# Kernel optimization log

Measured on AMD Instinct MI355X. Metric: run time of the kernel, lower is better.

The kernel has to match this reference:

```python
import jax, jax.numpy as jnp
import numpy as np

SE_TEMP = 0.2
BN_EPS = 1e-5

def _l2n(x):
    # F.normalize(p=2, dim=-1) with eps=1e-12 clamp on the norm
    n = jnp.linalg.norm(x, axis=-1, keepdims=True)
    return x / jnp.maximum(n, 1e-12)

def setup_inputs() -> dict:
    key = jax.random.key(0)
    k1, k2, k3, k4, k5 = jax.random.split(key, 5)
    Q, I, D = 256, 2048, 256
    return {
        "query_feats": jax.random.normal(k1, (Q, D), dtype=jnp.float32),
        "query_img_feats": jax.random.normal(k2, (Q, D), dtype=jnp.float32),
        "gallery_img_feats": jax.random.normal(k3, (I, D), dtype=jnp.float32),
        "bn_gamma": jnp.ones((D,), dtype=jnp.float32),
        "bn_beta": jnp.zeros((D,), dtype=jnp.float32),
        "bn_mean": jax.random.normal(k4, (D,), dtype=jnp.float32) * 0.1,
        "bn_var": jax.random.uniform(k5, (D,), dtype=jnp.float32, minval=0.5, maxval=1.5),
    }

def reference(query_feats, query_img_feats, gallery_img_feats, bn_gamma, bn_beta, bn_mean, bn_var):
    # GalleryFilterNetwork.get_scores, mode='combined', gfn_activation_mode='se'
    inv_std = bn_gamma / jnp.sqrt(bn_var + BN_EPS)

    def bn(x):  # eval-mode BatchNorm1d over last dim D
        return (x - bn_mean) * inv_std + bn_beta

    xq = _l2n(query_feats)        # [Q, D] normalized query box feats
    yq = _l2n(query_img_feats)    # [Q, D] normalized query scene feats
    yg = _l2n(gallery_img_feats)  # [I, D] normalized gallery scene feats

    gate = jax.nn.sigmoid(xq / SE_TEMP)           # [Q, D]
    fused_query = bn(yq * gate)                   # [Q, D]  (non-p SE fuse)
    fused_gal = bn(yg[:, None, :] * gate[None])   # [I, Q, D] (p=True SE fuse)

    # cosine similarity per (q, i) pair, then sigmoid
    scores = jax.nn.sigmoid(
        jnp.einsum('qd,iqd->qi', _l2n(fused_query), _l2n(fused_gal))
    )
    return scores  # [Q, I]
```

## Files before the change

kernel.cpp:

```cpp
#include <hip/hip_runtime.h>
#include <math.h>

#define D 256
#define Q 256
#define I 2048

typedef __attribute__((ext_vector_type(8))) short short8;
typedef __attribute__((ext_vector_type(4))) float floatx4;

__device__ __forceinline__ float sigmoidf_(float x) {
    return 1.0f / (1.0f + expf(-x));
}

__device__ __forceinline__ unsigned short f2bf(float f) {
    unsigned u = __float_as_uint(f);
    u += 0x7FFFu + ((u >> 16) & 1u);
    return (unsigned short)(u >> 16);
}

__device__ __forceinline__ float quad_sum(float v) {
    v += __shfl_xor(v, 16, 64);
    v += __shfl_xor(v, 32, 64);
    return v;
}

#define LOAD8(dst, src4, base)                                      \
    do {                                                            \
        float4 _a = (src4)[(base)];                                 \
        float4 _b = (src4)[(base) + 1];                             \
        (dst)[0] = _a.x; (dst)[1] = _a.y;                           \
        (dst)[2] = _a.z; (dst)[3] = _a.w;                           \
        (dst)[4] = _b.x; (dst)[5] = _b.y;                           \
        (dst)[6] = _b.z; (dst)[7] = _b.w;                           \
    } while (0)

__global__ void __launch_bounds__(64, 1)
gfn_one(const float* __restrict__ qf,
        const float* __restrict__ qif,
        const float* __restrict__ gal,
        const float* __restrict__ gamma,
        const float* __restrict__ beta,
        const float* __restrict__ mean,
        const float* __restrict__ var,
        float* __restrict__ out) {
    const int l = threadIdx.x;
    const int lm = l & 15, quad = l >> 4;
    const int q0 = blockIdx.x * 16, i0 = blockIdx.y * 32;
    const int qr = q0 + lm;
    const int cb = quad * 2;

    const float4* qf4  = (const float4*)qf;
    const float4* qif4 = (const float4*)qif;
    const float4* g4   = (const float4*)gal;
    const float4* ga4  = (const float4*)gamma;
    const float4* be4  = (const float4*)beta;
    const float4* me4  = (const float4*)mean;
    const float4* va4  = (const float4*)var;

    float xx[64];
#pragma unroll
    for (int ks = 0; ks < 8; ks++)
        LOAD8(&xx[ks * 8], qf4, qr * 64 + ks * 8 + cb);
    float nx = 0.f;
#pragma unroll
    for (int e = 0; e < 64; e++) nx += xx[e] * xx[e];
    nx = quad_sum(nx);
    const float inx = 1.0f / fmaxf(sqrtf(nx), 1e-12f);
#pragma unroll
    for (int e = 0; e < 64; e++) xx[e] = sigmoidf_(xx[e] * inx * 5.0f);

    float yy[64];
#pragma unroll
    for (int ks = 0; ks < 8; ks++)
        LOAD8(&yy[ks * 8], qif4, qr * 64 + ks * 8 + cb);
    float ny = 0.f;
#pragma unroll
    for (int e = 0; e < 64; e++) ny += yy[e] * yy[e];
    ny = quad_sum(ny);
    const float iny = 1.0f / fmaxf(sqrtf(ny), 1e-12f);

    float cc_[64];
#pragma unroll
    for (int ks = 0; ks < 8; ks++) {
        float pg[8], pb_[8], pm[8], pv[8];
        LOAD8(pg, ga4, ks * 8 + cb);
        LOAD8(pb_, be4, ks * 8 + cb);
        LOAD8(pm, me4, ks * 8 + cb);
        LOAD8(pv, va4, ks * 8 + cb);
#pragma unroll
        for (int e = 0; e < 8; e++) {
            const int j = ks * 8 + e;
            float is = pg[e] * rsqrtf(pv[e] + 1e-5f);
            float c = pb_[e] - pm[e] * is;
            float a = xx[j] * is;
            xx[j] = a;
            yy[j] = yy[j] * iny * a + c;
            cc_[j] = c;
        }
    }

    float nf = 0.f;
#pragma unroll
    for (int e = 0; e < 64; e++) nf += yy[e] * yy[e];
    nf = quad_sum(nf);
    const float inf_ = 1.0f / fmaxf(sqrtf(nf), 1e-12f);

    float s = 0.f, ccs = 0.f;
#pragma unroll
    for (int e = 0; e < 64; e++) {
        float u = yy[e] * inf_;
        s += u * cc_[e];
        ccs += cc_[e] * cc_[e];
    }
    const float sqv = quad_sum(s);
    const float ccv = quad_sum(ccs);

    short8 bp[8], bw[8], bv[8];
#pragma unroll
    for (int ks = 0; ks < 8; ks++) {
#pragma unroll
        for (int e = 0; e < 8; e++) {
            const int j = ks * 8 + e;
            float a = xx[j], c = cc_[j];
            float u = yy[j] * inf_;
            bp[ks][e] = (short)f2bf(u * a);
            bw[ks][e] = (short)f2bf(a * a);
            bv[ks][e] = (short)f2bf(2.0f * a * c);
        }
    }

#pragma unroll
    for (int it = 0; it < 2; it++) {
        const int ir = i0 + it * 16 + lm;
        float gv[64];
#pragma unroll
        for (int ks = 0; ks < 8; ks++)
            LOAD8(&gv[ks * 8], g4, (int)(ir * 64 + ks * 8 + cb));
        float nn = 0.f;
#pragma unroll
        for (int e = 0; e < 64; e++) nn += gv[e] * gv[e];
        nn = quad_sum(nn);
        const float inv = 1.0f / fmaxf(sqrtf(nn), 1e-12f);

        short8 ay[8], ay2[8];
#pragma unroll
        for (int ks = 0; ks < 8; ks++) {
#pragma unroll
            for (int e = 0; e < 8; e++) {
                float yv = gv[ks * 8 + e] * inv;
                ay[ks][e]  = (short)f2bf(yv);
                ay2[ks][e] = (short)f2bf(yv * yv);
            }
        }

        floatx4 acc1 = {0.f, 0.f, 0.f, 0.f};
        floatx4 acc2 = {0.f, 0.f, 0.f, 0.f};
#pragma unroll
        for (int ks = 0; ks < 8; ks++) {
            acc1 = __builtin_amdgcn_mfma_f32_16x16x32_bf16(ay[ks],  bp[ks], acc1, 0, 0, 0);
            acc2 = __builtin_amdgcn_mfma_f32_16x16x32_bf16(ay2[ks], bw[ks], acc2, 0, 0, 0);
            acc2 = __builtin_amdgcn_mfma_f32_16x16x32_bf16(ay[ks],  bv[ks], acc2, 0, 0, 0);
        }

        float4 o4;
        float* po = &o4.x;
#pragma unroll
        for (int rr = 0; rr < 4; rr++) {
            float nrm = fmaxf(sqrtf(fmaxf(acc2[rr] + ccv, 0.f)), 1e-12f);
            po[rr] = sigmoidf_((acc1[rr] + sqv) / nrm);
        }
        *(float4*)&out[(size_t)qr * I + i0 + it * 16 + quad * 4] = o4;
    }
}

extern "C" void kernel_launch(void* const* d_in, const int* in_sizes, int n_in,
                              void* d_out, int out_size, void* d_ws, size_t ws_size,
                              hipStream_t stream) {
    const float* qf    = (const float*)d_in[0];
    const float* qif   = (const float*)d_in[1];
    const float* gal   = (const float*)d_in[2];
    const float* gamma = (const float*)d_in[3];
    const float* beta  = (const float*)d_in[4];
    const float* mean  = (const float*)d_in[5];
    const float* var   = (const float*)d_in[6];
    float* out = (float*)d_out;

    gfn_one<<<dim3(Q / 16, I / 32), 64, 0, stream>>>(
        qf, qif, gal, gamma, beta, mean, var, out);
}
```

Measured before the change: 90.29 us.

## Share query prep across four waves via LDS and widen gallery tile

Blocks grow from one wave to four, and each block now covers 64 gallery rows instead of 32. The per-query preprocessing (normalization, sigmoid gate, BN fold, bf16 packing) is split so each wave handles 4 queries with 16 lanes per query. The results go into padded LDS tiles that all waves then read as MFMA B operands. This cuts how much query work is repeated per gallery row and how much each lane does, in exchange for an LDS round trip, a block barrier and more shared memory per block.

Result: faster. 78.84 us (-12.7%).

```diff
diff --git a/kernel.cpp b/kernel.cpp
--- a/kernel.cpp
+++ b/kernel.cpp
@@ -4,6 +4,7 @@
 #define D 256
 #define Q 256
 #define I 2048
+#define STRIDE 264
 
 typedef __attribute__((ext_vector_type(8))) short short8;
 typedef __attribute__((ext_vector_type(4))) float floatx4;
@@ -18,36 +19,37 @@
     return (unsigned short)(u >> 16);
 }
 
+__device__ __forceinline__ float grp16_sum(float v) {
+    v += __shfl_xor(v, 1, 64);
+    v += __shfl_xor(v, 2, 64);
+    v += __shfl_xor(v, 4, 64);
+    v += __shfl_xor(v, 8, 64);
+    return v;
+}
+
 __device__ __forceinline__ float quad_sum(float v) {
     v += __shfl_xor(v, 16, 64);
     v += __shfl_xor(v, 32, 64);
     return v;
 }
 
-#define LOAD8(dst, src4, base)                                      \
-    do {                                                            \
-        float4 _a = (src4)[(base)];                                 \
-        float4 _b = (src4)[(base) + 1];                             \
-        (dst)[0] = _a.x; (dst)[1] = _a.y;                           \
-        (dst)[2] = _a.z; (dst)[3] = _a.w;                           \
-        (dst)[4] = _b.x; (dst)[5] = _b.y;                           \
-        (dst)[6] = _b.z; (dst)[7] = _b.w;                           \
-    } while (0)
-
-__global__ void __launch_bounds__(64, 1)
-gfn_one(const float* __restrict__ qf,
-        const float* __restrict__ qif,
-        const float* __restrict__ gal,
-        const float* __restrict__ gamma,
-        const float* __restrict__ beta,
-        const float* __restrict__ mean,
-        const float* __restrict__ var,
-        float* __restrict__ out) {
-    const int l = threadIdx.x;
-    const int lm = l & 15, quad = l >> 4;
-    const int q0 = blockIdx.x * 16, i0 = blockIdx.y * 32;
-    const int qr = q0 + lm;
-    const int cb = quad * 2;
+__global__ void __launch_bounds__(256, 2)
+gfn_single(const float* __restrict__ qf,
+           const float* __restrict__ qif,
+           const float* __restrict__ gal,
+           const float* __restrict__ gamma,
+           const float* __restrict__ beta,
+           const float* __restrict__ mean,
+           const float* __restrict__ var,
+           float* __restrict__ out) {
+    __shared__ unsigned short sP[16 * STRIDE];
+    __shared__ unsigned short sW[16 * STRIDE];
+    __shared__ unsigned short sV[16 * STRIDE];
+    __shared__ float sq_s[16];
+
+    const int t = threadIdx.x;
+    const int w = t >> 6, l = t & 63;
+    const int q0 = blockIdx.x * 16, i0 = blockIdx.y * 64;
 
     const float4* qf4  = (const float4*)qf;
     const float4* qif4 = (const float4*)qif;
@@ -57,120 +59,157 @@
     const float4* me4  = (const float4*)mean;
     const float4* va4  = (const float4*)var;
 
-    float xx[64];
-#pragma unroll
-    for (int ks = 0; ks < 8; ks++)
-        LOAD8(&xx[ks * 8], qf4, qr * 64 + ks * 8 + cb);
+    const int grp = l >> 4, lj = l & 15;
+    const int qrow = w * 4 + grp;
+    const int q = q0 + qrow;
+
+    float4 xa[4], ya[4];
+#pragma unroll
+    for (int m = 0; m < 4; m++) xa[m] = qf4[q * 64 + lj * 4 + m];
     float nx = 0.f;
 #pragma unroll
-    for (int e = 0; e < 64; e++) nx += xx[e] * xx[e];
-    nx = quad_sum(nx);
+    for (int m = 0; m < 4; m++)
+        nx += xa[m].x * xa[m].x + xa[m].y * xa[m].y +
+              xa[m].z * xa[m].z + xa[m].w * xa[m].w;
+    nx = grp16_sum(nx);
     const float inx = 1.0f / fmaxf(sqrtf(nx), 1e-12f);
 #pragma unroll
-    for (int e = 0; e < 64; e++) xx[e] = sigmoidf_(xx[e] * inx * 5.0f);
-
-    float yy[64];
-#pragma unroll
-    for (int ks = 0; ks < 8; ks++)
-        LOAD8(&yy[ks * 8], qif4, qr * 64 + ks * 8 + cb);
+    for (int m = 0; m < 4; m++) {
+        xa[m].x = sigmoidf_(xa[m].x * inx * 5.0f);
+        xa[m].y = sigmoidf_(xa[m].y * inx * 5.0f);
+        xa[m].z = sigmoidf_(xa[m].z * inx * 5.0f);
+        xa[m].w = sigmoidf_(xa[m].w * inx * 5.0f);
+    }
+
+#pragma unroll
+    for (int m = 0; m < 4; m++) ya[m] = qif4[q * 64 + lj * 4 + m];
     float ny = 0.f;
 #pragma unroll
-    for (int e = 0; e < 64; e++) ny += yy[e] * yy[e];
-    ny = quad_sum(ny);
+    for (int m = 0; m < 4; m++)
+        ny += ya[m].x * ya[m].x + ya[m].y * ya[m].y +
+              ya[m].z * ya[m].z + ya[m].w * ya[m].w;
+    ny = grp16_sum(ny);
     const float iny = 1.0f / fmaxf(sqrtf(ny), 1e-12f);
 
-    float cc_[64];
+    float4 av[4], cv[4], fv[4];
+#pragma unroll
+    for (int m = 0; m < 4; m++) {
+        float4 g = ga4[lj * 4 + m], b = be4[lj * 4 + m];
+        float4 mn = me4[lj * 4 + m], vr = va4[lj * 4 + m];
+        float4 is, c, a, f;
+        is.x = g.x * rsqrtf(vr.x + 1e-5f);
+        is.y = g.y * rsqrtf(vr.y + 1e-5f);
+        is.z = g.z * rsqrtf(vr.z + 1e-5f);
+        is.w = g.w * rsqrtf(vr.w + 1e-5f);
+        c.x = b.x - mn.x * is.x;  c.y = b.y - mn.y * is.y;
+        c.z = b.z - mn.z * is.z;  c.w = b.w - mn.w * is.w;
+        a.x = xa[m].x * is.x;  a.y = xa[m].y * is.y;
+        a.z = xa[m].z * is.z;  a.w = xa[m].w * is.w;
+        f.x = ya[m].x * iny * a.x + c.x;
+        f.y = ya[m].y * iny * a.y + c.y;
+        f.z = ya[m].z * iny * a.z + c.z;
+        f.w = ya[m].w * iny * a.w + c.w;
+        av[m] = a; cv[m] = c; fv[m] = f;
+    }
+
+    float nf = 0.f;
+#pragma unroll
+    for (int m = 0; m < 4; m++)
+        nf += fv[m].x * fv[m].x + fv[m].y * fv[m].y +
+              fv[m].z * fv[m].z + fv[m].w * fv[m].w;
+    nf = grp16_sum(nf);
+    const float inf_ = 1.0f / fmaxf(sqrtf(nf), 1e-12f);
+
+    float s = 0.f, ccs = 0.f;
+    short8 hp[2], hw[2], hv[2];
+#pragma unroll
+    for (int m = 0; m < 4; m++) {
+        float4 u, a = av[m], c = cv[m];
+        u.x = fv[m].x * inf_; u.y = fv[m].y * inf_;
+        u.z = fv[m].z * inf_; u.w = fv[m].w * inf_;
+        s   += u.x * c.x + u.y * c.y + u.z * c.z + u.w * c.w;
+        ccs += c.x * c.x + c.y * c.y + c.z * c.z + c.w * c.w;
+        const int h = m >> 1, e0 = (m & 1) * 4;
+        hp[h][e0 + 0] = (short)f2bf(u.x * a.x);
+        hp[h][e0 + 1] = (short)f2bf(u.y * a.y);
+        hp[h][e0 + 2] = (short)f2bf(u.z * a.z);
+        hp[h][e0 + 3] = (short)f2bf(u.w * a.w);
+        hw[h][e0 + 0] = (short)f2bf(a.x * a.x);
+        hw[h][e0 + 1] = (short)f2bf(a.y * a.y);
+        hw[h][e0 + 2] = (short)f2bf(a.z * a.z);
+        hw[h][e0 + 3] = (short)f2bf(a.w * a.w);
+        hv[h][e0 + 0] = (short)f2bf(2.0f * a.x * c.x);
+        hv[h][e0 + 1] = (short)f2bf(2.0f * a.y * c.y);
+        hv[h][e0 + 2] = (short)f2bf(2.0f * a.z * c.z);
+        hv[h][e0 + 3] = (short)f2bf(2.0f * a.w * c.w);
+    }
+    s = grp16_sum(s);
+    const float ccv = grp16_sum(ccs);
+    if (lj == 0) sq_s[qrow] = s;
+
+    const int cb = qrow * STRIDE + lj * 16;
+    *(short8*)&sP[cb]     = hp[0];  *(short8*)&sP[cb + 8] = hp[1];
+    *(short8*)&sW[cb]     = hw[0];  *(short8*)&sW[cb + 8] = hw[1];
+    *(short8*)&sV[cb]     = hv[0];  *(short8*)&sV[cb + 8] = hv[1];
+
+    __syncthreads();
+
+    const int lm = l & 15, quad = l >> 4;
+    const int iw = i0 + w * 16;
+    const int ir = iw + lm;
+
+    float4 gva[16];
 #pragma unroll
     for (int ks = 0; ks < 8; ks++) {
-        float pg[8], pb_[8], pm[8], pv[8];
-        LOAD8(pg, ga4, ks * 8 + cb);
-        LOAD8(pb_, be4, ks * 8 + cb);
-        LOAD8(pm, me4, ks * 8 + cb);
-        LOAD8(pv, va4, ks * 8 + cb);
-#pragma unroll
-        for (int e = 0; e < 8; e++) {
-            const int j = ks * 8 + e;
-            float is = pg[e] * rsqrtf(pv[e] + 1e-5f);
-            float c = pb_[e] - pm[e] * is;
-            float a = xx[j] * is;
-            xx[j] = a;
-            yy[j] = yy[j] * iny * a + c;
-            cc_[j] = c;
-        }
-    }
-
-    float nf = 0.f;
-#pragma unroll
-    for (int e = 0; e < 64; e++) nf += yy[e] * yy[e];
-    nf = quad_sum(nf);
-    const float inf_ = 1.0f / fmaxf(sqrtf(nf), 1e-12f);
-
-    float s = 0.f, ccs = 0.f;
-#pragma unroll
-    for (int e = 0; e < 64; e++) {
-        float u = yy[e] * inf_;
-        s += u * cc_[e];
-        ccs += cc_[e] * cc_[e];
-    }
-    const float sqv = quad_sum(s);
-    const float ccv = quad_sum(ccs);
-
-    short8 bp[8], bw[8], bv[8];
+        gva[ks * 2]     = g4[ir * 64 + ks * 8 + quad * 2];
+        gva[ks * 2 + 1] = g4[ir * 64 + ks * 8 + quad * 2 + 1];
+    }
+    float nn = 0.f;
+#pragma unroll
+    for (int k = 0; k < 16; k++)
+        nn += gva[k].x * gva[k].x + gva[k].y * gva[k].y +
+              gva[k].z * gva[k].z + gva[k].w * gva[k].w;
+    nn = quad_sum(nn);
+    const float inv = 1.0f / fmaxf(sqrtf(nn), 1e-12f);
+
+    short8 ay[8], ay2[8];
 #pragma unroll
     for (int ks = 0; ks < 8; ks++) {
-#pragma unroll
-        for (int e = 0; e < 8; e++) {
-            const int j = ks * 8 + e;
-            float a = xx[j], c = cc_[j];
-            float u = yy[j] * inf_;
-            bp[ks][e] = (short)f2bf(u * a);
-            bw[ks][e] = (short)f2bf(a * a);
-            bv[ks][e] = (short)f2bf(2.0f * a * c);
-        }
-    }
-
-#pragma unroll
-    for (int it = 0; it < 2; it++) {
-        const int ir = i0 + it * 16 + lm;
-        float gv[64];
-#pragma unroll
-        for (int ks = 0; ks < 8; ks++)
-            LOAD8(&gv[ks * 8], g4, (int)(ir * 64 + ks * 8 + cb));
-        float nn = 0.f;
-#pragma unroll
-        for (int e = 0; e < 64; e++) nn += gv[e] * gv[e];
-        nn = quad_sum(nn);
-        const float inv = 1.0f / fmaxf(sqrtf(nn), 1e-12f);
-
-        short8 ay[8], ay2[8];
-#pragma unroll
-        for (int ks = 0; ks < 8; ks++) {
-#pragma unroll
-            for (int e = 0; e < 8; e++) {
-                float yv = gv[ks * 8 + e] * inv;
-                ay[ks][e]  = (short)f2bf(yv);
-                ay2[ks][e] = (short)f2bf(yv * yv);
-            }
-        }
-
-        floatx4 acc1 = {0.f, 0.f, 0.f, 0.f};
-        floatx4 acc2 = {0.f, 0.f, 0.f, 0.f};
-#pragma unroll
-        for (int ks = 0; ks < 8; ks++) {
-            acc1 = __builtin_amdgcn_mfma_f32_16x16x32_bf16(ay[ks],  bp[ks], acc1, 0, 0, 0);
-            acc2 = __builtin_amdgcn_mfma_f32_16x16x32_bf16(ay2[ks], bw[ks], acc2, 0, 0, 0);
-            acc2 = __builtin_amdgcn_mfma_f32_16x16x32_bf16(ay[ks],  bv[ks], acc2, 0, 0, 0);
-        }
-
-        float4 o4;
-        float* po = &o4.x;
-#pragma unroll
-        for (int rr = 0; rr < 4; rr++) {
-            float nrm = fmaxf(sqrtf(fmaxf(acc2[rr] + ccv, 0.f)), 1e-12f);
-            po[rr] = sigmoidf_((acc1[rr] + sqv) / nrm);
-        }
-        *(float4*)&out[(size_t)qr * I + i0 + it * 16 + quad * 4] = o4;
-    }
+        float4 A = gva[ks * 2], B = gva[ks * 2 + 1];
+        float y0 = A.x * inv, y1 = A.y * inv, y2 = A.z * inv, y3 = A.w * inv;
+        float y4 = B.x * inv, y5 = B.y * inv, y6 = B.z * inv, y7 = B.w * inv;
+        ay[ks][0] = (short)f2bf(y0);  ay[ks][1] = (short)f2bf(y1);
+        ay[ks][2] = (short)f2bf(y2);  ay[ks][3] = (short)f2bf(y3);
+        ay[ks][4] = (short)f2bf(y4);  ay[ks][5] = (short)f2bf(y5);
+        ay[ks][6] = (short)f2bf(y6);  ay[ks][7] = (short)f2bf(y7);
+        ay2[ks][0] = (short)f2bf(y0 * y0);  ay2[ks][1] = (short)f2bf(y1 * y1);
+        ay2[ks][2] = (short)f2bf(y2 * y2);  ay2[ks][3] = (short)f2bf(y3 * y3);
+        ay2[ks][4] = (short)f2bf(y4 * y4);  ay2[ks][5] = (short)f2bf(y5 * y5);
+        ay2[ks][6] = (short)f2bf(y6 * y6);  ay2[ks][7] = (short)f2bf(y7 * y7);
+    }
+
+    floatx4 acc1 = {0.f, 0.f, 0.f, 0.f};
+    floatx4 acc2 = {0.f, 0.f, 0.f, 0.f};
+#pragma unroll
+    for (int ks = 0; ks < 8; ks++) {
+        const int o = lm * STRIDE + ks * 32 + quad * 8;
+        short8 bp = *(const short8*)&sP[o];
+        short8 bw = *(const short8*)&sW[o];
+        short8 bv = *(const short8*)&sV[o];
+        acc1 = __builtin_amdgcn_mfma_f32_16x16x32_bf16(ay[ks],  bp, acc1, 0, 0, 0);
+        acc2 = __builtin_amdgcn_mfma_f32_16x16x32_bf16(ay2[ks], bw, acc2, 0, 0, 0);
+        acc2 = __builtin_amdgcn_mfma_f32_16x16x32_bf16(ay[ks],  bv, acc2, 0, 0, 0);
+    }
+
+    const float sqv = sq_s[lm];
+    float4 o4;
+    float* po = &o4.x;
+#pragma unroll
+    for (int rr = 0; rr < 4; rr++) {
+        float nrm = fmaxf(sqrtf(fmaxf(acc2[rr] + ccv, 0.f)), 1e-12f);
+        po[rr] = sigmoidf_((acc1[rr] + sqv) / nrm);
+    }
+    *(float4*)&out[(size_t)(q0 + lm) * I + iw + quad * 4] = o4;
 }
 
 extern "C" void kernel_launch(void* const* d_in, const int* in_sizes, int n_in,
@@ -185,6 +224,6 @@
     const float* var   = (const float*)d_in[6];
     float* out = (float*)d_out;
 
-    gfn_one<<<dim3(Q / 16, I / 32), 64, 0, stream>>>(
+    gfn_single<<<dim3(Q / 16, I / 64), 256, 0, stream>>>(
         qf, qif, gal, gamma, beta, mean, var, out);
 }
```
